# Optimization experiments

Measured on AMD Instinct MI355X. Metric: run time of the kernel, lower is better.

The kernel has to match this reference:

```python
import jax, jax.numpy as jnp
import numpy as np
import math

STRIDE = 32
CTR_CLAMP = 32.0
SCALE_CLAMP = math.log(1000.0 / 16)  # DEFAULT_SCALE_CLAMP
CONF_THRESH = 0.05
NMS_THRESH = 0.6
TOPK = 1000
NUM_CLASSES = 80
CLASS_OFFSET = 1.0e5  # separates classes so one IoU pass == per-class NMS


def setup_inputs() -> dict:
    key = jax.random.key(0)
    k1, k2 = jax.random.split(key)
    fmp_h, fmp_w = 100, 100
    A = 5
    M = fmp_h * fmp_w * A  # 50000 candidates
    cls_pred = jax.random.normal(k1, (M, NUM_CLASSES), dtype=jnp.float32)
    reg_pred = jax.random.normal(k2, (M, 4), dtype=jnp.float32)
    anchor_size = jnp.array([[32, 32], [64, 64], [128, 128], [256, 256], [512, 512]], dtype=jnp.float32)
    return {"cls_pred": cls_pred, "reg_pred": reg_pred, "anchor_size": anchor_size,
            "fmp_h": fmp_h, "fmp_w": fmp_w}


def _generate_anchors(anchor_size, fmp_h, fmp_w):
    # anchors laid out as [H*W, A, 4] -> [M, 4], matching torch.meshgrid order
    ys, xs = jnp.meshgrid(jnp.arange(fmp_h, dtype=jnp.float32),
                          jnp.arange(fmp_w, dtype=jnp.float32), indexing="ij")
    xy = (jnp.stack([xs, ys], axis=-1).reshape(-1, 2) + 0.5) * STRIDE  # [HW, 2]
    A = anchor_size.shape[0]
    anchor_xy = jnp.repeat(xy[:, None, :], A, axis=1)                   # [HW, A, 2]
    anchor_wh = jnp.broadcast_to(anchor_size[None], (xy.shape[0], A, 2))
    return jnp.concatenate([anchor_xy, anchor_wh], axis=-1).reshape(-1, 4)  # [M, 4]


def _decode_boxes(anchors, reg):
    # anchors/reg: [K, 4] (cx, cy, w, h) / (dx, dy, dw, dh)
    ctr_off = jnp.clip(reg[:, :2] * anchors[:, 2:], -CTR_CLAMP, CTR_CLAMP)
    ctr_xy = anchors[:, :2] + ctr_off
    wh = anchors[:, 2:] * jnp.exp(jnp.minimum(reg[:, 2:], SCALE_CLAMP))
    return jnp.concatenate([ctr_xy - 0.5 * wh, ctr_xy + 0.5 * wh], axis=-1)  # x1y1x2y2


def _greedy_nms_keep(boxes, valid):
    # boxes: [K, 4] already score-sorted descending; valid: [K] bool
    x1, y1, x2, y2 = boxes[:, 0], boxes[:, 1], boxes[:, 2], boxes[:, 3]
    areas = (x2 - x1) * (y2 - y1)
    xx1 = jnp.maximum(x1[:, None], x1[None, :])
    yy1 = jnp.maximum(y1[:, None], y1[None, :])
    xx2 = jnp.minimum(x2[:, None], x2[None, :])
    yy2 = jnp.minimum(y2[:, None], y2[None, :])
    inter = jnp.maximum(1e-28, xx2 - xx1) * jnp.maximum(1e-28, yy2 - yy1)
    iou = inter / (areas[:, None] + areas[None, :] - inter + 1e-14)  # [K, K]
    idxs = jnp.arange(boxes.shape[0])

    def body(i, keep):
        suppress = keep[i] & (iou[i] > NMS_THRESH) & (idxs > i)
        return keep & ~suppress

    return jax.lax.fori_loop(0, boxes.shape[0], body, valid)


def reference(cls_pred, reg_pred, anchor_size, fmp_h, fmp_w):
    anchors = _generate_anchors(anchor_size, fmp_h, fmp_w)  # [M, 4]
    probs = jax.nn.sigmoid(cls_pred)                        # [M, C]
    scores = probs.max(axis=-1)
    labels = probs.argmax(axis=-1)
    # top-k candidates (lax.top_k returns scores sorted descending)
    scores, idx = jax.lax.top_k(scores, TOPK)
    labels = labels[idx]
    reg = reg_pred[idx]
    anc = anchors[idx]
    boxes = _decode_boxes(anc, reg)                         # [K, 4] in pixels
    valid = scores >= CONF_THRESH
    # per-class NMS via class offsets (boxes of different classes never overlap)
    boxes_off = boxes + labels.astype(boxes.dtype)[:, None] * CLASS_OFFSET
    keep = _greedy_nms_keep(boxes_off, valid)
    img_w = fmp_w * STRIDE
    img_h = fmp_h * STRIDE
    scale = jnp.array([img_w, img_h, img_w, img_h], dtype=boxes.dtype)
    nboxes = jnp.clip(boxes / scale, 0.0, 1.0)
    m = keep.astype(boxes.dtype)
    return nboxes * m[:, None], scores * m, jnp.where(keep, labels, -1), keep
```

## Files before the change

kernel.cpp:

```cpp
#include <hip/hip_runtime.h>
#include <math.h>

#define NCLS 80
#define TOPK 1000
#define CAND_CAP 4096

__device__ __forceinline__ float sigmoid_np(float x) {
  float e = (float)exp(-(double)x);
  return 1.0f / (1.0f + e);
}
__device__ __forceinline__ float exp_np(float x) { return (float)exp((double)x); }

__device__ __forceinline__ unsigned fkey(float s) {
  unsigned u = __float_as_uint(s);
  return ((int)u < 0) ? ~u : (u | 0x80000000u);
}

#define KEY_BASE 0xBF000000u
__device__ __forceinline__ unsigned kbin(unsigned key) { return (key >> 11) & 0xFFFu; }

__device__ __forceinline__ void agg_add(unsigned* h, unsigned bin, bool pred) {
  unsigned long long rem = __ballot(pred);
  const int lane = threadIdx.x & 63;
  while (rem) {
    int leader = __ffsll(rem) - 1;
    unsigned lb = (unsigned)__shfl((int)bin, leader, 64);
    unsigned long long m = __ballot(pred && bin == lb);
    if (lane == leader) atomicAdd(&h[lb], (unsigned)__popcll(m));
    rem &= ~m;
  }
}

__global__ void k_zero(unsigned* __restrict__ p, int nwords) {
  int i = blockIdx.x * 256 + threadIdx.x;
  if (i < nwords) p[i] = 0u;
}

__launch_bounds__(1024)
__global__ void k_score(const float* __restrict__ cls, float* __restrict__ scores,
                        int* __restrict__ labels, unsigned* __restrict__ ghist1, int M) {
  __shared__ unsigned h1[4096];
  const int t = threadIdx.x;
  #pragma unroll
  for (int k = 0; k < 4; ++k) h1[t + 1024 * k] = 0u;
  __syncthreads();

  int gid = blockIdx.x * 1024 + t;
  int anchor = gid >> 2;
  int q = gid & 3;
  bool act = anchor < M;
  float lv[20];
  float best = -3.4e38f; int bc = 0;
  if (act) {
    const float4* row = reinterpret_cast<const float4*>(cls) + (size_t)anchor * (NCLS / 4);
    #pragma unroll
    for (int k = 0; k < 5; ++k) {
      float4 v = row[q + 4 * k];
      int cbase = (q + 4 * k) * 4;
      lv[4 * k + 0] = v.x; lv[4 * k + 1] = v.y; lv[4 * k + 2] = v.z; lv[4 * k + 3] = v.w;
      if (v.x > best) { best = v.x; bc = cbase + 0; }
      if (v.y > best) { best = v.y; bc = cbase + 1; }
      if (v.z > best) { best = v.z; bc = cbase + 2; }
      if (v.w > best) { best = v.w; bc = cbase + 3; }
    }
  } else {
    #pragma unroll
    for (int k = 0; k < 20; ++k) lv[k] = -3.4e38f;
  }
  #pragma unroll
  for (int d = 1; d < 4; d <<= 1) {
    float ob = __shfl_xor(best, d, 64);
    int oc = __shfl_xor(bc, d, 64);
    if (ob > best || (ob == best && oc < bc)) { best = ob; bc = oc; }
  }
  float s = sigmoid_np(best);
  float sp = s * (1.0f - s);
  float band = (s < 1.0f && sp > 0.0f) ? (4.8e-7f / sp) : 3.4e38f;
  float thresh = best - band;
  int cclose = 1 << 30;
  #pragma unroll
  for (int k = 0; k < 5; ++k) {
    #pragma unroll
    for (int j = 0; j < 4; ++j) {
      int c = (q + 4 * k) * 4 + j;
      if (lv[4 * k + j] >= thresh && c < cclose) cclose = c;
    }
  }
  #pragma unroll
  for (int d = 1; d < 4; d <<= 1) {
    int oc = __shfl_xor(cclose, d, 64);
    if (oc < cclose) cclose = oc;
  }
  int lab = bc;
  if (act && cclose < bc && q == 0) {
    float bp = -1.0f; int bl = 0;
    for (int c = 0; c < NCLS; ++c) {
      float p = sigmoid_np(cls[(size_t)anchor * NCLS + c]);
      if (p > bp) { bp = p; bl = c; }
    }
    lab = bl;
  }
  unsigned key = fkey(s);
  if (act && q == 0) {
    scores[anchor] = s;
    labels[anchor] = lab;
  }
  agg_add(h1, kbin(key), act && q == 0 && key >= KEY_BASE);
  __syncthreads();
  #pragma unroll
  for (int k = 0; k < 4; ++k) {
    unsigned c = h1[t + 1024 * k];
    if (c) atomicAdd(&ghist1[t + 1024 * k], c);
  }
}

__launch_bounds__(1024)
__global__ void k_select(const unsigned* __restrict__ ghist1, const float* __restrict__ scores,
                         const int* __restrict__ labels, const float* __restrict__ reg,
                         const float* __restrict__ asz, const int* __restrict__ pW,
                         int M, int A,
                         float* __restrict__ sel_score, int* __restrict__ sel_label,
                         float* __restrict__ boxes, float* __restrict__ areas,
                         float* __restrict__ obox) {
  __shared__ unsigned chunks[1024];
  __shared__ unsigned long long ck[CAND_CAP];
  __shared__ int sB1;
  __shared__ unsigned scnt;
  const int t = threadIdx.x;
  const int lane = t & 63;
  const int M4 = M >> 2;
  const float4* s4 = reinterpret_cast<const float4*>(scores);

  if (t == 0) { scnt = 0u; sB1 = 0; }

  unsigned hb0 = ghist1[4 * t], hb1 = ghist1[4 * t + 1],
           hb2 = ghist1[4 * t + 2], hb3 = ghist1[4 * t + 3];
  chunks[t] = hb0 + hb1 + hb2 + hb3;
  __syncthreads();
  for (int d = 1; d < 1024; d <<= 1) {
    unsigned v = chunks[t] + ((t + d < 1024) ? chunks[t + d] : 0u);
    __syncthreads(); chunks[t] = v; __syncthreads();
  }
  {
    unsigned ssc = chunks[t];
    unsigned ssn = (t + 1 < 1024) ? chunks[t + 1] : 0u;
    if (ssc >= (unsigned)TOPK && ssn < (unsigned)TOPK) {
      unsigned hb[4] = {hb0, hb1, hb2, hb3};
      unsigned run = ssn;
      for (int b = 3; b >= 0; --b) {
        run += hb[b];
        if (run >= (unsigned)TOPK) { sB1 = 4 * t + b; break; }
      }
    }
  }
  __syncthreads();
  const unsigned T = KEY_BASE + ((unsigned)sB1 << 11);

  #pragma unroll 2
  for (int i = t; i < M4; i += 1024) {
    float4 v = s4[i];
    unsigned kk[4] = {fkey(v.x), fkey(v.y), fkey(v.z), fkey(v.w)};
    #pragma unroll
    for (int j = 0; j < 4; ++j) {
      bool pred = kk[j] >= T;
      unsigned long long m = __ballot(pred);
      if (m) {
        int leader = __ffsll(m) - 1;
        unsigned base = 0;
        if (lane == leader) base = atomicAdd(&scnt, (unsigned)__popcll(m));
        base = (unsigned)__shfl((int)base, leader, 64);
        if (pred) {
          unsigned p = base + (unsigned)__popcll(m & ((1ull << lane) - 1ull));
          if (p < (unsigned)CAND_CAP)
            ck[p] = ((unsigned long long)kk[j] << 32) | (unsigned)(~(unsigned)(4 * i + j));
        }
      }
    }
  }
  for (int i = M4 * 4 + t; i < M; i += 1024) {
    unsigned key = fkey(scores[i]);
    if (key >= T) {
      unsigned p = atomicAdd(&scnt, 1u);
      if (p < (unsigned)CAND_CAP)
        ck[p] = ((unsigned long long)key << 32) | (unsigned)(~(unsigned)i);
    }
  }
  __syncthreads();
  unsigned n = scnt; if (n > (unsigned)CAND_CAP) n = (unsigned)CAND_CAP;

  for (int cc = 0; cc < CAND_CAP; cc += 1024) {
    if ((unsigned)cc >= n) break;
    int c = cc + t;
    bool actv = (unsigned)c < n;
    unsigned long long my = actv ? ck[c] : 0ull;
    int r = 0;
    for (int j = 0; j < (int)n; ++j) r += (ck[j] > my);
    if (actv && r < TOPK) {
      unsigned key = (unsigned)(my >> 32);
      unsigned u = (key & 0x80000000u) ? (key ^ 0x80000000u) : ~key;
      float scv = __uint_as_float(u);
      int idx = (int)(~(unsigned)my);
      int lab = labels[idx];
      int W = *pW;
      int a = idx % A;
      int cell = idx / A;
      int x = cell % W;
      int y = cell / W;
      float aw = asz[a * 2 + 0], ah = asz[a * 2 + 1];
      float ax = ((float)x + 0.5f) * 32.0f;
      float ay = ((float)y + 0.5f) * 32.0f;
      float4 rg = *reinterpret_cast<const float4*>(reg + (size_t)idx * 4);
      float offx = fminf(fmaxf(rg.x * aw, -32.0f), 32.0f);
      float offy = fminf(fmaxf(rg.y * ah, -32.0f), 32.0f);
      float cx = ax + offx, cy = ay + offy;
      const float SC = 4.135166556742356f;
      float bw = aw * exp_np(fminf(rg.z, SC));
      float bh = ah * exp_np(fminf(rg.w, SC));
      float x1 = cx - 0.5f * bw, y1 = cy - 0.5f * bh;
      float x2 = cx + 0.5f * bw, y2 = cy + 0.5f * bh;
      float off = (float)lab * 100000.0f;
      float ox1 = x1 + off, oy1 = y1 + off, ox2 = x2 + off, oy2 = y2 + off;
      sel_score[r] = scv; sel_label[r] = lab;
      boxes[r * 4 + 0] = x1; boxes[r * 4 + 1] = y1;
      boxes[r * 4 + 2] = x2; boxes[r * 4 + 3] = y2;
      obox[0 * 1024 + r] = ox1; obox[1 * 1024 + r] = oy1;
      obox[2 * 1024 + r] = ox2; obox[3 * 1024 + r] = oy2;
      areas[r] = (ox2 - ox1) * (oy2 - oy1);
    }
  }
}

__launch_bounds__(1024)
__global__ void k_mask(const float* __restrict__ obox, const float* __restrict__ areas,
                       unsigned long long* __restrict__ maskC) {
  __shared__ float so0[1024], so1[1024], so2[1024], so3[1024], sa[1024];
  const int t = threadIdx.x;
  const int c = blockIdx.x, j = t;
  so0[t] = obox[t];        so1[t] = obox[1024 + t];
  so2[t] = obox[2048 + t]; so3[t] = obox[3072 + t];
  sa[t] = areas[t];
  __syncthreads();
  unsigned long long bits = 0ull;
  if (j < TOPK) {
    float x1j = so0[j], y1j = so1[j], x2j = so2[j], y2j = so3[j];
    float aj = sa[j];
    int i0 = c * 64;
    for (int ii = 0; ii < 64; ++ii) {
      int i = i0 + ii;
      if (i < TOPK && i < j) {
        float xx1 = fmaxf(so0[i], x1j);
        float yy1 = fmaxf(so1[i], y1j);
        float xx2 = fminf(so2[i], x2j);
        float yy2 = fminf(so3[i], y2j);
        float inter = fmaxf(1e-28f, xx2 - xx1) * fmaxf(1e-28f, yy2 - yy1);
        float uni = sa[i] + aj - inter + 1e-14f;
        float iou = inter / uni;
        if (iou > 0.6f) bits |= (1ull << ii);
      }
    }
  }
  maskC[c * 1024 + j] = bits;
}

__launch_bounds__(512)
__global__ void k_nms(const unsigned long long* __restrict__ maskC,
                      const float* __restrict__ sel_score, const int* __restrict__ sel_label,
                      const float* __restrict__ boxes,
                      const int* __restrict__ pW, const int* __restrict__ pH,
                      float* __restrict__ out) {
  __shared__ unsigned long long sm[16 * 1024];
  __shared__ float ssc[1024];
  __shared__ unsigned long long kwS[16];
  const int tid = threadIdx.x;
  const int lane = tid & 63;

  {
    const float4* g4 = reinterpret_cast<const float4*>(maskC);
    float4* s4 = reinterpret_cast<float4*>(sm);
    float4 v[16];
    #pragma unroll
    for (int k = 0; k < 16; ++k) v[k] = g4[tid + k * 512];
    #pragma unroll
    for (int k = 0; k < 16; ++k) s4[tid + k * 512] = v[k];
  }
  #pragma unroll
  for (int k = 0; k < 2; ++k) {
    int i = tid + k * 512;
    ssc[i] = (i < TOPK) ? sel_score[i] : 0.0f;
  }
  __syncthreads();

  if (tid < 64) {
    unsigned long long supp[16];
    #pragma unroll
    for (int f = 0; f < 16; ++f) supp[f] = 0ull;
    #pragma unroll
    for (int f = 0; f < 16; ++f) {
      unsigned long long ct = sm[f * 1024 + f * 64 + lane];
      int r = f * 64 + lane;
      unsigned long long valid = __ballot((r < TOPK) && (ssc[r] >= 0.05f));
      unsigned long long sup_any = __ballot(ct != 0ull);
      unsigned long long avail = valid & ~supp[f];
      unsigned long long kwf = 0ull;
      while (avail) {
        unsigned long long fs = avail & sup_any;
        if (!fs) { kwf |= avail; break; }
        int i = __ffsll((long long)fs) - 1;
        unsigned long long below = (1ull << i) - 1ull;
        kwf |= avail & below;
        kwf |= (1ull << i);
        unsigned long long vict = __ballot(((ct >> i) & 1ull) != 0ull);
        avail &= ~vict;
        avail &= ~(below | (1ull << i));
      }
      if (lane == 0) kwS[f] = kwf;
      #pragma unroll
      for (int g = f + 1; g < 16; ++g)
        supp[g] |= __ballot((sm[f * 1024 + g * 64 + lane] & kwf) != 0ull);
    }
  }
  __syncthreads();

  float sw = (float)(*pW * 32);
  float sh = (float)(*pH * 32);
  const float4* b4 = reinterpret_cast<const float4*>(boxes);
  for (int r = tid; r < TOPK; r += 512) {
    bool kp = (kwS[r >> 6] >> (r & 63)) & 1ull;
    float m = kp ? 1.0f : 0.0f;
    float4 b = b4[r];
    float b0 = fminf(fmaxf(b.x / sw, 0.0f), 1.0f) * m;
    float b1 = fminf(fmaxf(b.y / sh, 0.0f), 1.0f) * m;
    float b2 = fminf(fmaxf(b.z / sw, 0.0f), 1.0f) * m;
    float b3 = fminf(fmaxf(b.w / sh, 0.0f), 1.0f) * m;
    out[r * 4 + 0] = b0; out[r * 4 + 1] = b1;
    out[r * 4 + 2] = b2; out[r * 4 + 3] = b3;
    out[TOPK * 4 + r] = ssc[r] * m;
    out[TOPK * 5 + r] = kp ? (float)sel_label[r] : -1.0f;
    out[TOPK * 6 + r] = m;
  }
}

extern "C" void kernel_launch(void* const* d_in, const int* in_sizes, int n_in,
                              void* d_out, int out_size, void* d_ws, size_t ws_size,
                              hipStream_t stream) {
  const float* cls = (const float*)d_in[0];
  const float* reg = (const float*)d_in[1];
  const float* asz = (const float*)d_in[2];
  const int* pH = (const int*)d_in[3];
  const int* pW = (const int*)d_in[4];
  int M = in_sizes[0] / NCLS;
  int A = in_sizes[2] / 2;

  char* ws = (char*)d_ws;
  size_t off = 0;
  auto alloc = [&](size_t bytes) { size_t o = off; off = (off + bytes + 255) & ~(size_t)255; return o; };
  size_t o_h1   = alloc(4096 * sizeof(unsigned));
  size_t o_sc   = alloc((size_t)M * sizeof(float));
  size_t o_lb   = alloc((size_t)M * sizeof(int));
  size_t o_ssc  = alloc(1024 * sizeof(float));
  size_t o_slb  = alloc(1024 * sizeof(int));
  size_t o_box  = alloc((size_t)TOPK * 4 * sizeof(float));
  size_t o_area = alloc(1024 * sizeof(float));
  size_t o_obox = alloc(4 * 1024 * sizeof(float));
  size_t o_mask = alloc((size_t)16 * 1024 * sizeof(unsigned long long));
  (void)ws_size; (void)out_size; (void)n_in;

  k_zero<<<16, 256, 0, stream>>>((unsigned*)(ws + o_h1), 4096);
  int nblk_score = (M * 4 + 1023) / 1024;
  k_score<<<nblk_score, 1024, 0, stream>>>(
      cls, (float*)(ws + o_sc), (int*)(ws + o_lb), (unsigned*)(ws + o_h1), M);
  k_select<<<1, 1024, 0, stream>>>(
      (const unsigned*)(ws + o_h1), (const float*)(ws + o_sc), (const int*)(ws + o_lb),
      reg, asz, pW, M, A,
      (float*)(ws + o_ssc), (int*)(ws + o_slb),
      (float*)(ws + o_box), (float*)(ws + o_area), (float*)(ws + o_obox));
  k_mask<<<16, 1024, 0, stream>>>(
      (const float*)(ws + o_obox), (const float*)(ws + o_area),
      (unsigned long long*)(ws + o_mask));
  k_nms<<<1, 512, 0, stream>>>(
      (const unsigned long long*)(ws + o_mask),
      (const float*)(ws + o_ssc), (const int*)(ws + o_slb),
      (const float*)(ws + o_box), pW, pH, (float*)d_out);
}
```

Measured before the change: 82.36 us.

## Split single-block top-k select into multi-block compaction and ranking kernels

The single-block selection kernel, which scanned all 50k scores to gather candidates above the histogram threshold, is split into two kernels. A multi-block compaction kernel has each block recompute the threshold from the histogram, then uses a wave prefix scan plus one global atomic per block to write candidates to a global buffer. A single-block rank kernel loads that buffer and does the rest as before. The goal is to spread the serial scan over many CUs, at the cost of an extra kernel launch, a redundant histogram scan in every block, and a global round trip for the candidates.

After: 74.49 us, median of 2. -9.6%, faster.

```diff
diff --git a/kernel.cpp b/kernel.cpp
--- a/kernel.cpp
+++ b/kernel.cpp
@@ -115,23 +115,16 @@
 }
 
 __launch_bounds__(1024)
-__global__ void k_select(const unsigned* __restrict__ ghist1, const float* __restrict__ scores,
-                         const int* __restrict__ labels, const float* __restrict__ reg,
-                         const float* __restrict__ asz, const int* __restrict__ pW,
-                         int M, int A,
-                         float* __restrict__ sel_score, int* __restrict__ sel_label,
-                         float* __restrict__ boxes, float* __restrict__ areas,
-                         float* __restrict__ obox) {
+__global__ void k_compact(const unsigned* __restrict__ ghist1, const float* __restrict__ scores,
+                          unsigned long long* __restrict__ cand, unsigned* __restrict__ gcount,
+                          int M) {
   __shared__ unsigned chunks[1024];
-  __shared__ unsigned long long ck[CAND_CAP];
   __shared__ int sB1;
-  __shared__ unsigned scnt;
+  __shared__ unsigned wcnt[16];
+  __shared__ unsigned sbase;
   const int t = threadIdx.x;
-  const int lane = t & 63;
-  const int M4 = M >> 2;
-  const float4* s4 = reinterpret_cast<const float4*>(scores);
-
-  if (t == 0) { scnt = 0u; sB1 = 0; }
+  const int lane = t & 63, wid = t >> 6;
+  if (t == 0) sB1 = 0;
 
   unsigned hb0 = ghist1[4 * t], hb1 = ghist1[4 * t + 1],
            hb2 = ghist1[4 * t + 2], hb3 = ghist1[4 * t + 3];
@@ -156,38 +149,54 @@
   __syncthreads();
   const unsigned T = KEY_BASE + ((unsigned)sB1 << 11);
 
-  #pragma unroll 2
-  for (int i = t; i < M4; i += 1024) {
-    float4 v = s4[i];
+  int base = (blockIdx.x * 1024 + t) * 4;
+  unsigned keys[4]; int idxs[4]; int np = 0;
+  if (base + 3 < M) {
+    float4 v = *reinterpret_cast<const float4*>(scores + base);
     unsigned kk[4] = {fkey(v.x), fkey(v.y), fkey(v.z), fkey(v.w)};
     #pragma unroll
-    for (int j = 0; j < 4; ++j) {
-      bool pred = kk[j] >= T;
-      unsigned long long m = __ballot(pred);
-      if (m) {
-        int leader = __ffsll(m) - 1;
-        unsigned base = 0;
-        if (lane == leader) base = atomicAdd(&scnt, (unsigned)__popcll(m));
-        base = (unsigned)__shfl((int)base, leader, 64);
-        if (pred) {
-          unsigned p = base + (unsigned)__popcll(m & ((1ull << lane) - 1ull));
-          if (p < (unsigned)CAND_CAP)
-            ck[p] = ((unsigned long long)kk[j] << 32) | (unsigned)(~(unsigned)(4 * i + j));
-        }
-      }
-    }
-  }
-  for (int i = M4 * 4 + t; i < M; i += 1024) {
-    unsigned key = fkey(scores[i]);
-    if (key >= T) {
-      unsigned p = atomicAdd(&scnt, 1u);
-      if (p < (unsigned)CAND_CAP)
-        ck[p] = ((unsigned long long)key << 32) | (unsigned)(~(unsigned)i);
-    }
-  }
-  __syncthreads();
-  unsigned n = scnt; if (n > (unsigned)CAND_CAP) n = (unsigned)CAND_CAP;
-
+    for (int j = 0; j < 4; ++j)
+      if (kk[j] >= T) { keys[np] = kk[j]; idxs[np] = base + j; ++np; }
+  } else {
+    for (int i = base; i < M; ++i) {
+      unsigned key = fkey(scores[i]);
+      if (key >= T) { keys[np] = key; idxs[np] = i; ++np; }
+    }
+  }
+  int sc = np;
+  #pragma unroll
+  for (int d = 1; d < 64; d <<= 1) {
+    int o = __shfl_up(sc, d, 64);
+    if (lane >= d) sc += o;
+  }
+  if (lane == 63) wcnt[wid] = (unsigned)sc;
+  __syncthreads();
+  if (t == 0) {
+    unsigned acc = 0;
+    for (int w = 0; w < 16; ++w) { unsigned v = wcnt[w]; wcnt[w] = acc; acc += v; }
+    sbase = acc ? atomicAdd(gcount, acc) : 0u;
+  }
+  __syncthreads();
+  unsigned pos = sbase + wcnt[wid] + (unsigned)(sc - np);
+  for (int j = 0; j < np; ++j) {
+    if (pos < (unsigned)CAND_CAP)
+      cand[pos] = ((unsigned long long)keys[j] << 32) | (unsigned)(~(unsigned)idxs[j]);
+    ++pos;
+  }
+}
+
+__launch_bounds__(1024)
+__global__ void k_rank(const unsigned long long* __restrict__ cand, const unsigned* __restrict__ gcount,
+                       const int* __restrict__ labels, const float* __restrict__ reg,
+                       const float* __restrict__ asz, const int* __restrict__ pW, int A,
+                       float* __restrict__ sel_score, int* __restrict__ sel_label,
+                       float* __restrict__ boxes, float* __restrict__ areas,
+                       float* __restrict__ obox) {
+  __shared__ unsigned long long ck[CAND_CAP];
+  const int t = threadIdx.x;
+  unsigned n = *gcount; if (n > (unsigned)CAND_CAP) n = (unsigned)CAND_CAP;
+  for (int i = t; i < (int)n; i += 1024) ck[i] = cand[i];
+  __syncthreads();
   for (int cc = 0; cc < CAND_CAP; cc += 1024) {
     if ((unsigned)cc >= n) break;
     int c = cc + t;
@@ -355,6 +364,9 @@
   size_t off = 0;
   auto alloc = [&](size_t bytes) { size_t o = off; off = (off + bytes + 255) & ~(size_t)255; return o; };
   size_t o_h1   = alloc(4096 * sizeof(unsigned));
+  size_t o_cnt  = alloc(256);
+  size_t zero_end = off;
+  size_t o_cand = alloc((size_t)CAND_CAP * sizeof(unsigned long long));
   size_t o_sc   = alloc((size_t)M * sizeof(float));
   size_t o_lb   = alloc((size_t)M * sizeof(int));
   size_t o_ssc  = alloc(1024 * sizeof(float));
@@ -365,13 +377,18 @@
   size_t o_mask = alloc((size_t)16 * 1024 * sizeof(unsigned long long));
   (void)ws_size; (void)out_size; (void)n_in;
 
-  k_zero<<<16, 256, 0, stream>>>((unsigned*)(ws + o_h1), 4096);
+  int zwords = (int)(zero_end / 4);
+  k_zero<<<(zwords + 255) / 256, 256, 0, stream>>>((unsigned*)ws, zwords);
   int nblk_score = (M * 4 + 1023) / 1024;
   k_score<<<nblk_score, 1024, 0, stream>>>(
       cls, (float*)(ws + o_sc), (int*)(ws + o_lb), (unsigned*)(ws + o_h1), M);
-  k_select<<<1, 1024, 0, stream>>>(
-      (const unsigned*)(ws + o_h1), (const float*)(ws + o_sc), (const int*)(ws + o_lb),
-      reg, asz, pW, M, A,
+  int nblk_cmp = ((M + 3) / 4 + 1023) / 1024;
+  k_compact<<<nblk_cmp, 1024, 0, stream>>>(
+      (const unsigned*)(ws + o_h1), (const float*)(ws + o_sc),
+      (unsigned long long*)(ws + o_cand), (unsigned*)(ws + o_cnt), M);
+  k_rank<<<1, 1024, 0, stream>>>(
+      (const unsigned long long*)(ws + o_cand), (const unsigned*)(ws + o_cnt),
+      (const int*)(ws + o_lb), reg, asz, pW, A,
       (float*)(ws + o_ssc), (int*)(ws + o_slb),
       (float*)(ws + o_box), (float*)(ws + o_area), (float*)(ws + o_obox));
   k_mask<<<16, 1024, 0, stream>>>(
```
